# Performance work log

Measured on AMD Instinct MI355X. Metric: run time of the kernel, lower is better.

Reference implementation:

```python
import jax, jax.numpy as jnp
import numpy as np

N, M, D, H = 256, 1024, 512, 512


def setup_inputs() -> dict:
    key = jax.random.key(0)
    k1, k2, k3, k4 = jax.random.split(key, 4)
    scale = 1.0 / np.sqrt(D)
    return {
        "embeddings": jax.random.normal(k1, (N, D), dtype=jnp.float32),
        "support_tensors": jax.random.normal(k2, (M, D), dtype=jnp.float32),
        "W1": jax.random.normal(k3, (D, H), dtype=jnp.float32) * scale,
        "b1": jnp.zeros((H,), dtype=jnp.float32),
        "W2": jax.random.normal(k4, (H, 1), dtype=jnp.float32) * (1.0 / np.sqrt(H)),
        "b2": jnp.zeros((1,), dtype=jnp.float32),
    }


def reference(embeddings, support_tensors, W1, b1, W2, b2):
    # SupportLayer.call: tile queries x support set into all N*M pairs,
    # apply pairwise kernel (siamese head: sigmoid(MLP(|a - b|))),
    # reshape back to similarity matrix [N, M].
    # Broadcasting replaces the explicit tf.tile / reshape.
    diff = jnp.abs(embeddings[:, None, :] - support_tensors[None, :, :])  # [N, M, D]
    h = jax.nn.relu(jnp.einsum("nmd,dh->nmh", diff, W1) + b1)             # [N, M, H]
    logits = jnp.einsum("nmh,ho->nmo", h, W2)[..., 0] + b2[0]             # [N, M]
    return jax.nn.sigmoid(logits)
```

## Files before the change

### kernel.cpp

```cpp
#include <hip/hip_runtime.h>
#include <hip/hip_bf16.h>

#define N_Q 256
#define M_S 1024
#define DD 512
#define HH 512

typedef __attribute__((ext_vector_type(8))) short short8;
typedef __attribute__((ext_vector_type(8))) __bf16 bf16x8;
typedef __attribute__((ext_vector_type(16))) float f32x16;
typedef __attribute__((ext_vector_type(2))) __bf16 bf16x2;

union U8 { short8 s; bf16x8 b; };

__device__ __forceinline__ unsigned short f2bf(float f) {
  unsigned int u = __float_as_uint(f);
  u += 0x7FFFu + ((u >> 16) & 1u);
  return (unsigned short)(u >> 16);
}

__device__ __forceinline__ short8 pack8(const float* d) {
#if defined(__has_builtin) && __has_builtin(__builtin_amdgcn_cvt_pk_bf16_f32)
  short8 r;
#pragma unroll
  for (int i = 0; i < 4; ++i) {
    union { bf16x2 v; short s[2]; } u;
    u.v = __builtin_amdgcn_cvt_pk_bf16_f32(d[2 * i], d[2 * i + 1]);
    r[2 * i] = u.s[0];
    r[2 * i + 1] = u.s[1];
  }
  return r;
#else
  short8 r;
#pragma unroll
  for (int i = 0; i < 8; ++i) r[i] = (short)f2bf(d[i]);
  return r;
#endif
}

__device__ __forceinline__ short8 packdiff(float4 e0, float4 e1, float4 s0, float4 s1) {
  float d[8];
  d[0] = fabsf(e0.x - s0.x); d[1] = fabsf(e0.y - s0.y);
  d[2] = fabsf(e0.z - s0.z); d[3] = fabsf(e0.w - s0.w);
  d[4] = fabsf(e1.x - s1.x); d[5] = fabsf(e1.y - s1.y);
  d[6] = fabsf(e1.z - s1.z); d[7] = fabsf(e1.w - s1.w);
  return pack8(d);
}

__global__ __launch_bounds__(512) void prep_w1s(const float* __restrict__ W1,
                                                unsigned short* __restrict__ w1s) {
  const int f = blockIdx.x;
  const int kc = f >> 4, h32 = f & 15;
  const int l = threadIdx.x & 63, j = threadIdx.x >> 6;
  const int h = h32 * 32 + (l & 31);
  const int k = kc * 16 + (l >> 5) * 8 + j;
  w1s[f * 512 + l * 8 + j] = f2bf(W1[k * HH + h]);
}

__global__ __launch_bounds__(1024, 4) void support_kernel(
    const float* __restrict__ emb, const float* __restrict__ sup,
    const unsigned short* __restrict__ w1s, const float* __restrict__ b1,
    const float* __restrict__ W2, const float* __restrict__ b2,
    float* __restrict__ out) {
  extern __shared__ short8 As16[];

  const int tid = threadIdx.x;
  const int lane = tid & 63;
  const int wid = tid >> 6;
  const int l31 = lane & 31;
  const int khalf = lane >> 5;
  const int hslice = wid & 7;
  const int pgset = wid >> 3;

  const int m0 = blockIdx.x * 16;
  const int n0 = blockIdx.y * 8;

  const int c = tid & 63;
  const int rg = tid >> 6;
  const int nl = rg >> 1;
  const int mq = rg & 1;

  const unsigned short* bb = w1s + (hslice * 2) * 512 + lane * 8;
  U8 b[3][2];
#pragma unroll
  for (int tj = 0; tj < 2; ++tj) {
    b[0][tj].s = *(const short8*)(bb + (0 * 16 + tj) * 512);
    b[1][tj].s = *(const short8*)(bb + (1 * 16 + tj) * 512);
  }

  {
    const float* ep = emb + (n0 + nl) * DD + c * 8;
    const float4 e0 = *(const float4*)ep;
    const float4 e1 = *(const float4*)(ep + 4);
    const float* sbase = sup + (m0 + mq * 8) * DD + c * 8;
#pragma unroll
    for (int j = 0; j < 8; ++j) {
      const float4 s0 = *(const float4*)(sbase + j * DD);
      const float4 s1 = *(const float4*)(sbase + j * DD + 4);
      const int p = rg * 8 + j;
      As16[p * 64 + (c ^ j)] = packdiff(e0, e1, s0, s1);
    }
  }
  __syncthreads();

  const int ar0 = (pgset * 64 + 0 + l31) * 64;
  const int ar1 = (pgset * 64 + 32 + l31) * 64;
  const int ax = l31 & 7;

  f32x16 acc[2][2] = {};
  U8 a[2][2];
  a[0][0].s = As16[ar0 + (khalf ^ ax)];
  a[0][1].s = As16[ar1 + (khalf ^ ax)];

#pragma unroll
  for (int ks = 0; ks < 32; ++ks) {
    const int cur = ks & 1;
    if (ks < 31) {
      const int cc = ((ks + 1) * 2 + khalf) ^ ax;
      a[cur ^ 1][0].s = As16[ar0 + cc];
      a[cur ^ 1][1].s = As16[ar1 + cc];
    }
    if (ks + 2 < 32) {
#pragma unroll
      for (int tj = 0; tj < 2; ++tj)
        b[(ks + 2) % 3][tj].s = *(const short8*)(bb + ((ks + 2) * 16 + tj) * 512);
    }
    __builtin_amdgcn_s_setprio(1);
#pragma unroll
    for (int am = 0; am < 2; ++am)
#pragma unroll
      for (int tj = 0; tj < 2; ++tj)
        acc[am][tj] = __builtin_amdgcn_mfma_f32_32x32x16_bf16(
            b[ks % 3][tj].b, a[cur][am].b, acc[am][tj], 0, 0, 0);
    __builtin_amdgcn_s_setprio(0);
  }

  float s[2];
#pragma unroll
  for (int am = 0; am < 2; ++am) {
    float sm = 0.f;
#pragma unroll
    for (int tj = 0; tj < 2; ++tj) {
      const float* b1p = b1 + (hslice * 2 + tj) * 32 + khalf * 4;
      const float* w2p = W2 + (hslice * 2 + tj) * 32 + khalf * 4;
#pragma unroll
      for (int rq = 0; rq < 4; ++rq) {
        const float4 b1q = *(const float4*)(b1p + rq * 8);
        const float4 w2q = *(const float4*)(w2p + rq * 8);
        sm += fmaxf(acc[am][tj][rq * 4 + 0] + b1q.x, 0.f) * w2q.x;
        sm += fmaxf(acc[am][tj][rq * 4 + 1] + b1q.y, 0.f) * w2q.y;
        sm += fmaxf(acc[am][tj][rq * 4 + 2] + b1q.z, 0.f) * w2q.z;
        sm += fmaxf(acc[am][tj][rq * 4 + 3] + b1q.w, 0.f) * w2q.w;
      }
    }
    sm += __shfl_xor(sm, 32, 64);
    s[am] = sm;
  }
  __syncthreads();
  float* psums = (float*)As16;
  psums[(pgset * 64 + lane) * 9 + hslice] = khalf ? s[1] : s[0];
  __syncthreads();
  if (tid < 128) {
    float t = b2[0];
#pragma unroll
    for (int w = 0; w < 8; ++w) t += psums[tid * 9 + w];
    out[(n0 + (tid >> 4)) * M_S + m0 + (tid & 15)] = 1.f / (1.f + __expf(-t));
  }
}

extern "C" void kernel_launch(void* const* d_in, const int* in_sizes, int n_in,
                              void* d_out, int out_size, void* d_ws, size_t ws_size,
                              hipStream_t stream) {
  const float* emb = (const float*)d_in[0];
  const float* sup = (const float*)d_in[1];
  const float* W1  = (const float*)d_in[2];
  const float* b1  = (const float*)d_in[3];
  const float* W2  = (const float*)d_in[4];
  const float* b2  = (const float*)d_in[5];
  float* out = (float*)d_out;
  unsigned short* w1s = (unsigned short*)d_ws;

  static bool attr_done = false;
  if (!attr_done) {
    hipFuncSetAttribute((const void*)support_kernel,
                        hipFuncAttributeMaxDynamicSharedMemorySize, 131072);
    attr_done = true;
  }

  prep_w1s<<<512, 512, 0, stream>>>(W1, w1s);
  support_kernel<<<dim3(M_S / 16, N_Q / 8), 1024, 131072, stream>>>(
      emb, sup, w1s, b1, W2, b2, out);
}
```

Baseline: 212.7 us.

## Halve block to 8 waves, each computing 4x2 MFMA tiles over all pairs

The support kernel drops from 1024 threads (16 waves split across two pair groups) to 512 threads, where each wave covers all 128 query-support pairs of the block for its H slice. Every W1 fragment loaded from global memory now feeds 8 MFMAs instead of 4, which halves W1 traffic per block. The difference-tile build and the partial-sum reduction are remapped to match. In exchange, accumulator register pressure doubles and the CU runs half as many waves to hide LDS and global latency.

Result: faster. 185.7 us (-12.7%).

```diff
diff --git a/kernel.cpp b/kernel.cpp
--- a/kernel.cpp
+++ b/kernel.cpp
@@ -57,7 +57,7 @@
   w1s[f * 512 + l * 8 + j] = f2bf(W1[k * HH + h]);
 }
 
-__global__ __launch_bounds__(1024, 4) void support_kernel(
+__global__ __launch_bounds__(512, 2) void support_kernel(
     const float* __restrict__ emb, const float* __restrict__ sup,
     const unsigned short* __restrict__ w1s, const float* __restrict__ b1,
     const float* __restrict__ W2, const float* __restrict__ b2,
@@ -69,18 +69,11 @@
   const int wid = tid >> 6;
   const int l31 = lane & 31;
   const int khalf = lane >> 5;
-  const int hslice = wid & 7;
-  const int pgset = wid >> 3;
 
   const int m0 = blockIdx.x * 16;
   const int n0 = blockIdx.y * 8;
 
-  const int c = tid & 63;
-  const int rg = tid >> 6;
-  const int nl = rg >> 1;
-  const int mq = rg & 1;
-
-  const unsigned short* bb = w1s + (hslice * 2) * 512 + lane * 8;
+  const unsigned short* bb = w1s + (wid * 2) * 512 + lane * 8;
   U8 b[3][2];
 #pragma unroll
   for (int tj = 0; tj < 2; ++tj) {
@@ -89,28 +82,37 @@
   }
 
   {
-    const float* ep = emb + (n0 + nl) * DD + c * 8;
+    const int c = tid & 63;
+    const int rg = tid >> 6;
+    const float* ep = emb + (n0 + rg) * DD + c * 8;
     const float4 e0 = *(const float4*)ep;
     const float4 e1 = *(const float4*)(ep + 4);
-    const float* sbase = sup + (m0 + mq * 8) * DD + c * 8;
-#pragma unroll
-    for (int j = 0; j < 8; ++j) {
+    const float* sbase = sup + m0 * DD + c * 8;
+#pragma unroll
+    for (int j = 0; j < 16; ++j) {
       const float4 s0 = *(const float4*)(sbase + j * DD);
       const float4 s1 = *(const float4*)(sbase + j * DD + 4);
-      const int p = rg * 8 + j;
-      As16[p * 64 + (c ^ j)] = packdiff(e0, e1, s0, s1);
+      const int p = rg * 16 + j;
+      As16[p * 64 + (c ^ (j & 7))] = packdiff(e0, e1, s0, s1);
     }
   }
   __syncthreads();
 
-  const int ar0 = (pgset * 64 + 0 + l31) * 64;
-  const int ar1 = (pgset * 64 + 32 + l31) * 64;
   const int ax = l31 & 7;
-
-  f32x16 acc[2][2] = {};
-  U8 a[2][2];
-  a[0][0].s = As16[ar0 + (khalf ^ ax)];
-  a[0][1].s = As16[ar1 + (khalf ^ ax)];
+  const int ar0 = (0 * 32 + l31) * 64;
+  const int ar1 = (1 * 32 + l31) * 64;
+  const int ar2 = (2 * 32 + l31) * 64;
+  const int ar3 = (3 * 32 + l31) * 64;
+
+  f32x16 acc[4][2] = {};
+  U8 a[2][4];
+  {
+    const int c0 = khalf ^ ax;
+    a[0][0].s = As16[ar0 + c0];
+    a[0][1].s = As16[ar1 + c0];
+    a[0][2].s = As16[ar2 + c0];
+    a[0][3].s = As16[ar3 + c0];
+  }
 
 #pragma unroll
   for (int ks = 0; ks < 32; ++ks) {
@@ -119,6 +121,8 @@
       const int cc = ((ks + 1) * 2 + khalf) ^ ax;
       a[cur ^ 1][0].s = As16[ar0 + cc];
       a[cur ^ 1][1].s = As16[ar1 + cc];
+      a[cur ^ 1][2].s = As16[ar2 + cc];
+      a[cur ^ 1][3].s = As16[ar3 + cc];
     }
     if (ks + 2 < 32) {
 #pragma unroll
@@ -127,7 +131,7 @@
     }
     __builtin_amdgcn_s_setprio(1);
 #pragma unroll
-    for (int am = 0; am < 2; ++am)
+    for (int am = 0; am < 4; ++am)
 #pragma unroll
       for (int tj = 0; tj < 2; ++tj)
         acc[am][tj] = __builtin_amdgcn_mfma_f32_32x32x16_bf16(
@@ -135,30 +139,39 @@
     __builtin_amdgcn_s_setprio(0);
   }
 
-  float s[2];
-#pragma unroll
-  for (int am = 0; am < 2; ++am) {
-    float sm = 0.f;
+  float s0a, s1a, s2a, s3a;
+  {
+    float sm[4] = {0.f, 0.f, 0.f, 0.f};
 #pragma unroll
     for (int tj = 0; tj < 2; ++tj) {
-      const float* b1p = b1 + (hslice * 2 + tj) * 32 + khalf * 4;
-      const float* w2p = W2 + (hslice * 2 + tj) * 32 + khalf * 4;
+      const float* b1p = b1 + (wid * 2 + tj) * 32 + khalf * 4;
+      const float* w2p = W2 + (wid * 2 + tj) * 32 + khalf * 4;
 #pragma unroll
       for (int rq = 0; rq < 4; ++rq) {
         const float4 b1q = *(const float4*)(b1p + rq * 8);
         const float4 w2q = *(const float4*)(w2p + rq * 8);
-        sm += fmaxf(acc[am][tj][rq * 4 + 0] + b1q.x, 0.f) * w2q.x;
-        sm += fmaxf(acc[am][tj][rq * 4 + 1] + b1q.y, 0.f) * w2q.y;
-        sm += fmaxf(acc[am][tj][rq * 4 + 2] + b1q.z, 0.f) * w2q.z;
-        sm += fmaxf(acc[am][tj][rq * 4 + 3] + b1q.w, 0.f) * w2q.w;
+#pragma unroll
+        for (int am = 0; am < 4; ++am) {
+          sm[am] += fmaxf(acc[am][tj][rq * 4 + 0] + b1q.x, 0.f) * w2q.x;
+          sm[am] += fmaxf(acc[am][tj][rq * 4 + 1] + b1q.y, 0.f) * w2q.y;
+          sm[am] += fmaxf(acc[am][tj][rq * 4 + 2] + b1q.z, 0.f) * w2q.z;
+          sm[am] += fmaxf(acc[am][tj][rq * 4 + 3] + b1q.w, 0.f) * w2q.w;
+        }
       }
     }
-    sm += __shfl_xor(sm, 32, 64);
-    s[am] = sm;
+#pragma unroll
+    for (int am = 0; am < 4; ++am) sm[am] += __shfl_xor(sm[am], 32, 64);
+    s0a = sm[0]; s1a = sm[1]; s2a = sm[2]; s3a = sm[3];
   }
   __syncthreads();
   float* psums = (float*)As16;
-  psums[(pgset * 64 + lane) * 9 + hslice] = khalf ? s[1] : s[0];
+  {
+    const float v0 = khalf ? s2a : s0a;
+    const float v1 = khalf ? s3a : s1a;
+    const int p0 = khalf * 64 + l31;
+    psums[p0 * 9 + wid] = v0;
+    psums[(p0 + 32) * 9 + wid] = v1;
+  }
   __syncthreads();
   if (tid < 128) {
     float t = b2[0];
@@ -188,6 +201,6 @@
   }
 
   prep_w1s<<<512, 512, 0, stream>>>(W1, w1s);
-  support_kernel<<<dim3(M_S / 16, N_Q / 8), 1024, 131072, stream>>>(
+  support_kernel<<<dim3(M_S / 16, N_Q / 8), 512, 131072, stream>>>(
       emb, sup, w1s, b1, W2, b2, out);
 }
```
